# Performance work log

Measured on AMD Instinct MI355X. Metric: run time of the kernel, lower is better.

## Reference

```python
import math
import jax, jax.numpy as jnp
import numpy as np

PE_DIM = 128
NUM_HEADS = 8
U = V = 2
TEMP = 10000.0


def sine_pe(y_embed, x_embed, num_pos_feats, temperature, card):
    """Matches get_sine_position_encoding with use_norm=True."""
    eps = 1e-6
    scale = 2.0 * math.pi
    y = y_embed / (card[0] + eps) * scale
    x = x_embed / (card[1] + eps) * scale
    dim_t = jnp.asarray(temperature, jnp.float32) ** (
        2.0 * (jnp.arange(num_pos_feats, dtype=jnp.float32) // 2) / num_pos_feats)
    px = x[..., None] / dim_t
    py = y[..., None] / dim_t

    def interleave(p):
        s = jnp.sin(p[..., 0::2])
        c = jnp.cos(p[..., 1::2])
        return jnp.stack((s, c), axis=-1).reshape(p.shape[:-1] + (-1,))

    return jnp.concatenate((interleave(py), interleave(px)), axis=-1)


def setup_inputs() -> dict:
    key = jax.random.key(0)
    ks = jax.random.split(key, 8)
    B, C, H, W = 2, 64, 256, 256
    dim = C
    # xavier-ish scale for Linear(128 -> 64)
    w_std = math.sqrt(2.0 / (PE_DIM + dim))
    return {
        "feat_supp": jax.random.normal(ks[0], (B, C, H, W), jnp.float32),
        "flow": jax.random.normal(ks[1], (B, H, W, 2), jnp.float32) * 3.0,
        "feat_curr": jax.random.normal(ks[2], (B, C, H, W), jnp.float32),
        "q_w": jax.random.normal(ks[3], (dim, PE_DIM), jnp.float32) * w_std,
        "q_b": jnp.zeros((dim,), jnp.float32),
        "k_w": jax.random.normal(ks[4], (dim, PE_DIM), jnp.float32) * w_std,
        "k_b": jnp.zeros((dim,), jnp.float32),
        "v_w": jax.random.normal(ks[5], (dim, PE_DIM), jnp.float32) * w_std,
        "v_b": jnp.zeros((dim,), jnp.float32),
    }


def reference(feat_supp, flow, feat_curr, q_w, q_b, k_w, k_b, v_w, v_b):
    B, C, H, W = feat_curr.shape
    UV = U * V
    HW = H * W
    nh = NUM_HEADS
    hd = C // nh
    d = PE_DIM // C  # pe channels per feature channel
    scale = hd ** (-0.5)

    # flow-displaced integer grid + fractional part
    img_off = jnp.stack(
        jnp.meshgrid(jnp.arange(H), jnp.arange(W), indexing="ij"), axis=-1
    ).astype(flow.dtype)                                   # (H, W, 2) in (y, x)
    grid_full = img_off[None] + flow[..., ::-1]            # flow flipped to (y, x)
    grid_intg = jnp.floor(grid_full).astype(jnp.int32)
    grid_deci = grid_full - grid_intg                      # (B, H, W, 2)

    win_off = jnp.stack(
        jnp.meshgrid(jnp.arange(U), jnp.arange(V), indexing="ij"), axis=-1
    ).astype(jnp.int32)                                    # (U, V, 2)
    grid_w = grid_intg[:, :, :, None, None, :] + win_off[None, None, None]
    grid_w = grid_w.reshape(B, HW * UV, 2)
    deci = grid_deci.reshape(B, HW, 2)

    # duplicate-padding gather of support features
    h_idx = jnp.clip(grid_w[..., 0], 0, H - 1)
    w_idx = jnp.clip(grid_w[..., 1], 0, W - 1)
    lin = h_idx * W + w_idx                                # (B, HW*UV)
    feat_warp = jnp.take_along_axis(
        feat_supp.reshape(B, C, HW), lin[:, None, :], axis=2)  # (B, C, HW*UV)
    feat_warp = feat_warp.transpose(0, 2, 1).reshape(B, HW, UV, C)

    # window position bias (card = window_size - 1, use_corrected_card=False)
    wy, wx = jnp.meshgrid(jnp.arange(U, dtype=jnp.float32),
                          jnp.arange(V, dtype=jnp.float32), indexing="ij")
    pos_bias = sine_pe(wy.reshape(1, -1), wx.reshape(1, -1),
                       PE_DIM // 2, TEMP, (U - 1, V - 1))   # (1, UV, PE_DIM)
    pe_warp = pos_bias.reshape(1, 1, UV, C, d)
    fw = (feat_warp[..., None] + pe_warp).reshape(B, HW, UV, PE_DIM)

    # current-frame features + fractional-offset positional encoding
    fc = feat_curr.reshape(B, C, HW).transpose(0, 2, 1)     # (B, HW, C)
    pe_curr = sine_pe(deci[..., 0], deci[..., 1],
                      PE_DIM // 2, TEMP, (U, V))            # (B, HW, PE_DIM)
    fc = (fc[..., None] + pe_curr.reshape(B, HW, C, d)).reshape(B, HW, PE_DIM)

    q = (fc @ q_w.T + q_b).reshape(B, HW, nh, hd)
    k = (fw @ k_w.T + k_b).reshape(B, HW, UV, nh, hd)
    v = (fw @ v_w.T + v_b).reshape(B, HW, UV, nh, hd)

    attn = jnp.einsum("bnhd,bnuhd->bnhu", q * scale, k)
    attn = jax.nn.softmax(attn, axis=-1)
    out = jnp.einsum("bnhu,bnuhd->bnhd", attn, v).reshape(B, HW, C)
    return out.reshape(B, H, W, C).transpose(0, 3, 1, 2)
```

## Files before the change

### kernel.cpp

```cpp
#include <hip/hip_runtime.h>
#include <hip/hip_bf16.h>

#define HWHW 65536
#define LN1E4_32 0.28782313662425572f
#define TWO_PI_N 6.2831847f

typedef __attribute__((ext_vector_type(8))) short short8;
typedef __attribute__((ext_vector_type(4))) short s16x4;
typedef __attribute__((ext_vector_type(4))) float f32x4;


__device__ __forceinline__ short f2bf(float f) {
  union { __hip_bfloat16 h; short s; } u;
  u.h = __float2bfloat16(f);
  return u.s;
}

__global__ __launch_bounds__(256)
void pre_pass(const float* __restrict__ supp,
              const float* __restrict__ qw, const float* __restrict__ kw,
              const float* __restrict__ vw,
              const float* __restrict__ kb, const float* __restrict__ vb,
              __hip_bfloat16* __restrict__ suppT,
              __hip_bfloat16* __restrict__ wfrag, float* __restrict__ bias) {
  const int t = threadIdx.x;
  if (blockIdx.x < 2048) {
    __shared__ short tile[64 * 68];
    const int b   = blockIdx.x >> 10;
    const int p0  = (blockIdx.x & 1023) << 6;
    const int px4 = (t & 15) << 2;
    const int g   = t >> 4;

    const float* src = supp + ((size_t)b * 64 + g * 4) * HWHW + p0 + px4;
    f32x4 v[4];
#pragma unroll
    for (int c = 0; c < 4; ++c)
      v[c] = *(const f32x4*)(src + (size_t)c * HWHW);
#pragma unroll
    for (int j = 0; j < 4; ++j) {
      s16x4 pk;
#pragma unroll
      for (int c = 0; c < 4; ++c) pk[c] = f2bf(v[c][j]);
      *(s16x4*)&tile[(px4 + j) * 68 + g * 4] = pk;
    }
    __syncthreads();
    const int px = t >> 2, ch0 = (t & 3) << 4;
    s16x4 r0 = *(s16x4*)&tile[px * 68 + ch0];
    s16x4 r1 = *(s16x4*)&tile[px * 68 + ch0 + 4];
    s16x4 r2 = *(s16x4*)&tile[px * 68 + ch0 + 8];
    s16x4 r3 = *(s16x4*)&tile[px * 68 + ch0 + 12];
    short8 o0, o1;
#pragma unroll
    for (int j = 0; j < 4; ++j) {
      o0[j] = r0[j]; o0[j + 4] = r1[j];
      o1[j] = r2[j]; o1[j + 4] = r3[j];
    }
    short8* dst = (short8*)(suppT + ((size_t)(b * HWHW + p0 + px)) * 64 + ch0);
    dst[0] = o0;
    dst[1] = o1;
  } else if (blockIdx.x < 2056) {
    int slot = (blockIdx.x - 2048) * 256 + t;
    __hip_bfloat16* dst = wfrag + slot * 8;
    if (slot < 1024) {
      int ksnt = slot >> 6, lane = slot & 63;
      int ks = ksnt >> 2, nt = ksnt & 3;
      const float* w = qw + (nt * 16 + (lane & 15)) * 128 + ks * 32 + (lane >> 4) * 8;
#pragma unroll
      for (int j = 0; j < 8; ++j) dst[j] = __float2bfloat16(w[j]);
    } else {
      int mat = (slot >= 1536);
      int rem = slot & 511;
      int ksnt = rem >> 6, lane = rem & 63;
      int ks = ksnt >> 2, nt = ksnt & 3;
      int c0 = ks * 32 + (lane >> 4) * 8;
      const float* w = (mat ? vw : kw) + (nt * 16 + (lane & 15)) * 128;
#pragma unroll
      for (int j = 0; j < 8; ++j)
        dst[j] = __float2bfloat16(w[2 * (c0 + j)] + w[2 * (c0 + j) + 1]);
    }
  } else {
    for (int s = t; s < 512; s += 256) {
      int mat = s >> 8, uv = (s >> 6) & 3, c = s & 63;
      const float* w = (mat ? vw : kw) + c * 128;
      float acc = (mat ? vb : kb)[c];
      for (int kk = 0; kk < 128; ++kk) {
        float val = (kk < 64 ? (float)(uv >> 1) : (float)(uv & 1)) * TWO_PI_N;
        int i = kk & 63, f = i >> 1;
        float arg = val * __expf(-(float)f * LN1E4_32);
        float pe = (i & 1) ? __cosf(arg) : __sinf(arg);
        acc += pe * w[kk];
      }
      bias[s] = acc;
    }
  }
}

__global__ __attribute__((amdgpu_waves_per_eu(3, 5))) __launch_bounds__(256)
void iw_main(const __hip_bfloat16* __restrict__ suppT, const float* __restrict__ flow,
             const float* __restrict__ feat_curr,
             const short8* __restrict__ wg, const float* __restrict__ bias_g,
             const float* __restrict__ q_b, float* __restrict__ out)
{
  __shared__ float outstage[64 * 65];

  const int tid = threadIdx.x;
  const int idx = ((blockIdx.x & 7) << 8) | (blockIdx.x >> 3);
  const int b   = idx >> 10;
  const int hw0 = (idx & 1023) << 6;
  const int lane = tid & 63, wv = tid >> 6;
  const int quad = lane >> 4, l15 = lane & 15;

  float invd[2][4];
#pragma unroll
  for (int a = 0; a < 2; ++a)
#pragma unroll
    for (int jj = 0; jj < 4; ++jj)
      invd[a][jj] = __expf(-(float)(a * 16 + quad * 4 + jj) * LN1E4_32);

  f32x4 qacc[4];
  {
    short8 qwf[16];
#pragma unroll
    for (int i = 0; i < 16; ++i) qwf[i] = wg[i * 64 + lane];

    const int qpix = hw0 + wv * 16 + l15;
    float2 fl = ((const float2*)flow)[b * HWHW + qpix];
    float gy = (float)(qpix >> 8) + fl.y;
    float gx = (float)(qpix & 255) + fl.x;
    float vy = (gy - floorf(gy)) * (6.2831853071795864f / 2.000001f);
    float vx = (gx - floorf(gx)) * (6.2831853071795864f / 2.000001f);

    short8 qa[4];
#pragma unroll
    for (int ks = 0; ks < 4; ++ks) {
      float val = (ks < 2) ? vy : vx;
#pragma unroll
      for (int jj = 0; jj < 4; ++jj) {
        int c = ks * 16 + quad * 4 + jj;
        float feat = feat_curr[(b * 64 + c) * HWHW + qpix];
        float arg = val * invd[ks & 1][jj];
        qa[ks][jj * 2]     = f2bf(feat + __sinf(arg));
        qa[ks][jj * 2 + 1] = f2bf(feat + __cosf(arg));
      }
    }
#pragma unroll
    for (int nt = 0; nt < 4; ++nt) qacc[nt] = (f32x4){0.f, 0.f, 0.f, 0.f};
#pragma unroll
    for (int ks = 0; ks < 4; ++ks)
#pragma unroll
      for (int nt = 0; nt < 4; ++nt)
        qacc[nt] = __builtin_amdgcn_mfma_f32_16x16x32_bf16(
            qa[ks], qwf[ks * 4 + nt], qacc[nt], 0, 0, 0);
  }

  float qT[4][4];
  {
#pragma unroll
    for (int nt = 0; nt < 4; ++nt) {
      float qb = q_b[nt * 16 + l15];
#pragma unroll
      for (int r = 0; r < 4; ++r)
        qacc[nt][r] = (qacc[nt][r] + qb) * 0.35355339059327373f;
    }
#pragma unroll
    for (int mt = 0; mt < 4; ++mt)
#pragma unroll
      for (int nt = 0; nt < 4; ++nt) {
        int src = mt * 16 + l15;
        float v0 = __shfl(qacc[nt][0], src);
        float v1 = __shfl(qacc[nt][1], src);
        float v2 = __shfl(qacc[nt][2], src);
        float v3 = __shfl(qacc[nt][3], src);
        float t0 = (quad & 2) ? v2 : v0;
        float t1 = (quad & 2) ? v3 : v1;
        qT[mt][nt] = (quad & 1) ? t1 : t0;
      }
  }

  float kbr[4][4], vbr[4][4];
#pragma unroll
  for (int r = 0; r < 4; ++r)
#pragma unroll
    for (int nt = 0; nt < 4; ++nt) {
      kbr[r][nt] = bias_g[r * 64 + nt * 16 + l15];
      vbr[r][nt] = bias_g[256 + r * 64 + nt * 16 + l15];
    }

  short8 kf[8], vf[8];
#pragma unroll
  for (int i = 0; i < 8; ++i) {
    kf[i] = wg[1024 + i * 64 + lane];
    vf[i] = wg[1536 + i * 64 + lane];
  }

  const int uvl  = l15 & 3;
  const int prow = l15 >> 2;
  const short8* sT = (const short8*)suppT;

#pragma unroll
  for (int mt = 0; mt < 4; ++mt) {
    const int gpix = hw0 + wv * 16 + mt * 4 + prow;
    float2 fl = ((const float2*)flow)[b * HWHW + gpix];
    float fy = fl.y + (float)(gpix >> 8);
    float fx = fl.x + (float)(gpix & 255);
    int yy = min(max((int)floorf(fy) + (uvl >> 1), 0), 255);
    int xx = min(max((int)floorf(fx) + (uvl & 1), 0), 255);
    size_t base = (size_t)(b * HWHW + yy * 256 + xx) * 8;

    short8 ka0 = sT[base + quad];
    short8 ka1 = sT[base + 4 + quad];

    f32x4 kacc[4], vacc[4];
#pragma unroll
    for (int nt = 0; nt < 4; ++nt) {
      kacc[nt] = (f32x4){0.f, 0.f, 0.f, 0.f};
      vacc[nt] = (f32x4){0.f, 0.f, 0.f, 0.f};
    }
#pragma unroll
    for (int nt = 0; nt < 4; ++nt) {
      kacc[nt] = __builtin_amdgcn_mfma_f32_16x16x32_bf16(ka0, kf[nt],     kacc[nt], 0, 0, 0);
      vacc[nt] = __builtin_amdgcn_mfma_f32_16x16x32_bf16(ka0, vf[nt],     vacc[nt], 0, 0, 0);
      kacc[nt] = __builtin_amdgcn_mfma_f32_16x16x32_bf16(ka1, kf[4 + nt], kacc[nt], 0, 0, 0);
      vacc[nt] = __builtin_amdgcn_mfma_f32_16x16x32_bf16(ka1, vf[4 + nt], vacc[nt], 0, 0, 0);
    }

#pragma unroll
    for (int nt = 0; nt < 4; ++nt) {
      float lg[4];
#pragma unroll
      for (int r = 0; r < 4; ++r) {
        float p = qT[mt][nt] * (kacc[nt][r] + kbr[r][nt]);
        p += __shfl_xor(p, 1);
        p += __shfl_xor(p, 2);
        p += __shfl_xor(p, 4);
        lg[r] = p;
      }
      float mx = fmaxf(fmaxf(lg[0], lg[1]), fmaxf(lg[2], lg[3]));
      float e0 = __expf(lg[0] - mx), e1 = __expf(lg[1] - mx);
      float e2 = __expf(lg[2] - mx), e3 = __expf(lg[3] - mx);
      float inv = 1.0f / (e0 + e1 + e2 + e3);
      float o = (e0 * (vacc[nt][0] + vbr[0][nt]) + e1 * (vacc[nt][1] + vbr[1][nt]) +
                 e2 * (vacc[nt][2] + vbr[2][nt]) + e3 * (vacc[nt][3] + vbr[3][nt])) * inv;
      outstage[(nt * 16 + l15) * 65 + wv * 16 + mt * 4 + quad] = o;
    }
  }

  __syncthreads();
#pragma unroll
  for (int i = 0; i < 16; ++i) {
    int j = i * 256 + tid;
    int c = j >> 6, p = j & 63;
    out[(b * 64 + c) * HWHW + hw0 + p] = outstage[c * 65 + p];
  }
}

extern "C" void kernel_launch(void* const* d_in, const int* in_sizes, int n_in,
                              void* d_out, int out_size, void* d_ws, size_t ws_size,
                              hipStream_t stream) {
  const float* feat_supp = (const float*)d_in[0];
  const float* flow      = (const float*)d_in[1];
  const float* feat_curr = (const float*)d_in[2];
  const float* q_w = (const float*)d_in[3];
  const float* q_b = (const float*)d_in[4];
  const float* k_w = (const float*)d_in[5];
  const float* k_b = (const float*)d_in[6];
  const float* v_w = (const float*)d_in[7];
  const float* v_b = (const float*)d_in[8];
  float* out = (float*)d_out;
  (void)in_sizes; (void)n_in; (void)out_size; (void)ws_size;

  __hip_bfloat16* wfrag = (__hip_bfloat16*)d_ws;
  float* bias           = (float*)((char*)d_ws + 32768);
  __hip_bfloat16* suppT = (__hip_bfloat16*)((char*)d_ws + 65536);

  hipLaunchKernelGGL(pre_pass, dim3(2057), dim3(256), 0, stream,
                     feat_supp, q_w, k_w, v_w, k_b, v_b, suppT, wfrag, bias);
  hipLaunchKernelGGL(iw_main, dim3(2048), dim3(256), 0, stream,
                     suppT, flow, feat_curr, (const short8*)d_ws, bias, q_b, out);
}
```

Baseline: 181.6 us.

## Prefetch warped support gathers early and reuse query-pass integer flow via shuffles

The per-tile reload of flow and the floor computation for the gather addresses are removed. The integer grid already computed in the query pass is broadcast with lane shuffles instead. The first two tiles' support gathers are issued before the Q MFMAs, and later tiles are double-buffered so each gather overlaps the previous tile's MFMA work. This hides gather latency in exchange for more live registers, which may affect occupancy.

```diff
diff --git a/kernel.cpp b/kernel.cpp
--- a/kernel.cpp
+++ b/kernel.cpp
@@ -109,6 +109,9 @@
   const int hw0 = (idx & 1023) << 6;
   const int lane = tid & 63, wv = tid >> 6;
   const int quad = lane >> 4, l15 = lane & 15;
+  const int uvl  = l15 & 3;
+  const int prow = l15 >> 2;
+  const short8* sT = (const short8*)suppT;
 
   float invd[2][4];
 #pragma unroll
@@ -117,7 +120,10 @@
     for (int jj = 0; jj < 4; ++jj)
       invd[a][jj] = __expf(-(float)(a * 16 + quad * 4 + jj) * LN1E4_32);
 
+  int iy, ix;
+  short8 ka[2][2];
   f32x4 qacc[4];
+
   {
     short8 qwf[16];
 #pragma unroll
@@ -127,8 +133,10 @@
     float2 fl = ((const float2*)flow)[b * HWHW + qpix];
     float gy = (float)(qpix >> 8) + fl.y;
     float gx = (float)(qpix & 255) + fl.x;
-    float vy = (gy - floorf(gy)) * (6.2831853071795864f / 2.000001f);
-    float vx = (gx - floorf(gx)) * (6.2831853071795864f / 2.000001f);
+    float fy = floorf(gy), fx = floorf(gx);
+    iy = (int)fy; ix = (int)fx;
+    float vy = (gy - fy) * (6.2831853071795864f / 2.000001f);
+    float vx = (gx - fx) * (6.2831853071795864f / 2.000001f);
 
     short8 qa[4];
 #pragma unroll
@@ -143,6 +151,17 @@
         qa[ks][jj * 2 + 1] = f2bf(feat + __cosf(arg));
       }
     }
+
+#pragma unroll
+    for (int pm = 0; pm < 2; ++pm) {
+      int p  = pm * 4 + prow;
+      int yy = min(max(__shfl(iy, p) + (uvl >> 1), 0), 255);
+      int xx = min(max(__shfl(ix, p) + (uvl & 1), 0), 255);
+      size_t base = (size_t)(b * HWHW + yy * 256 + xx) * 8;
+      ka[pm][0] = sT[base + quad];
+      ka[pm][1] = sT[base + 4 + quad];
+    }
+
 #pragma unroll
     for (int nt = 0; nt < 4; ++nt) qacc[nt] = (f32x4){0.f, 0.f, 0.f, 0.f};
 #pragma unroll
@@ -193,22 +212,10 @@
     vf[i] = wg[1536 + i * 64 + lane];
   }
 
-  const int uvl  = l15 & 3;
-  const int prow = l15 >> 2;
-  const short8* sT = (const short8*)suppT;
-
 #pragma unroll
   for (int mt = 0; mt < 4; ++mt) {
-    const int gpix = hw0 + wv * 16 + mt * 4 + prow;
-    float2 fl = ((const float2*)flow)[b * HWHW + gpix];
-    float fy = fl.y + (float)(gpix >> 8);
-    float fx = fl.x + (float)(gpix & 255);
-    int yy = min(max((int)floorf(fy) + (uvl >> 1), 0), 255);
-    int xx = min(max((int)floorf(fx) + (uvl & 1), 0), 255);
-    size_t base = (size_t)(b * HWHW + yy * 256 + xx) * 8;
-
-    short8 ka0 = sT[base + quad];
-    short8 ka1 = sT[base + 4 + quad];
+    short8 ka0 = ka[mt & 1][0];
+    short8 ka1 = ka[mt & 1][1];
 
     f32x4 kacc[4], vacc[4];
 #pragma unroll
@@ -222,6 +229,15 @@
       vacc[nt] = __builtin_amdgcn_mfma_f32_16x16x32_bf16(ka0, vf[nt],     vacc[nt], 0, 0, 0);
       kacc[nt] = __builtin_amdgcn_mfma_f32_16x16x32_bf16(ka1, kf[4 + nt], kacc[nt], 0, 0, 0);
       vacc[nt] = __builtin_amdgcn_mfma_f32_16x16x32_bf16(ka1, vf[4 + nt], vacc[nt], 0, 0, 0);
+    }
+
+    if (mt < 2) {
+      int p  = (mt + 2) * 4 + prow;
+      int yy = min(max(__shfl(iy, p) + (uvl >> 1), 0), 255);
+      int xx = min(max(__shfl(ix, p) + (uvl & 1), 0), 255);
+      size_t base = (size_t)(b * HWHW + yy * 256 + xx) * 8;
+      ka[mt & 1][0] = sT[base + quad];
+      ka[mt & 1][1] = sT[base + 4 + quad];
     }
 
 #pragma unroll
```

Measured after the change: 229.7 us. 26.5% more time.
